# Kernel optimization log

Hardware: AMD Instinct MI355X
Metric: run time of the kernel (lower is better)

The kernel has to match this reference:

```python
import jax, jax.numpy as jnp
import numpy as np

B, L, DM, H = 1, 2048, 3072, 24
D = DM // H            # 128 head dim
MLP = 4 * DM           # 12288
EPS = 1e-6


def setup_inputs() -> dict:
    key = jax.random.key(0)
    ks = jax.random.split(key, 12)
    s = lambda fan_in: 1.0 / np.sqrt(fan_in)
    return {
        "x": jax.random.normal(ks[0], (B, L, DM), jnp.float32),
        "vec": jax.random.normal(ks[1], (B, DM), jnp.float32),
        "pe": jax.random.normal(ks[2], (1, 1, L, D // 2, 2, 2), jnp.float32),
        # Modulation linear: dim -> 3*dim
        "mod_w": jax.random.normal(ks[3], (DM, 3 * DM), jnp.float32) * s(DM),
        "mod_b": jnp.zeros((3 * DM,), jnp.float32),
        # linear1: dim -> 3*dim + mlp
        "lin1_w": jax.random.normal(ks[4], (DM, 3 * DM + MLP), jnp.float32) * s(DM),
        "lin1_b": jnp.zeros((3 * DM + MLP,), jnp.float32),
        # linear2: dim + mlp -> dim
        "lin2_w": jax.random.normal(ks[5], (DM + MLP, DM), jnp.float32) * s(DM + MLP),
        "lin2_b": jnp.zeros((DM,), jnp.float32),
        # QKNorm RMS scales (per head_dim)
        "q_scale": jnp.ones((D,), jnp.float32),
        "k_scale": jnp.ones((D,), jnp.float32),
    }


def _rms_norm(t, scale):
    # RMSNorm over last dim (head_dim), eps 1e-6
    rrms = jax.lax.rsqrt(jnp.mean(jnp.square(t), axis=-1, keepdims=True) + EPS)
    return t * rrms * scale


def _apply_rope(t, pe):
    # t: (B,H,L,D); pe: (1,1,L,D/2,2,2) as in flux apply_rope
    t2 = t.reshape(B, H, L, D // 2, 1, 2)
    out = pe[..., 0] * t2[..., 0] + pe[..., 1] * t2[..., 1]  # (B,H,L,D/2,2)
    return out.reshape(B, H, L, D)


def reference(x, vec, pe, mod_w, mod_b, lin1_w, lin1_b, lin2_w, lin2_b, q_scale, k_scale):
    # Modulation: Linear(silu(vec)) -> shift, scale, gate, each (B,1,DM)
    mod = jax.nn.silu(vec) @ mod_w + mod_b
    shift, scale, gate = jnp.split(mod[:, None, :], 3, axis=-1)

    # pre_norm: LayerNorm without affine, eps 1e-6
    mu = jnp.mean(x, axis=-1, keepdims=True)
    var = jnp.mean(jnp.square(x - mu), axis=-1, keepdims=True)
    xn = (x - mu) * jax.lax.rsqrt(var + EPS)
    x_mod = (1.0 + scale) * xn + shift

    # fused QKV + MLP projection
    h = x_mod @ lin1_w + lin1_b
    qkv, mlp = h[..., : 3 * DM], h[..., 3 * DM :]
    qkv = qkv.reshape(B, L, 3, H, D).transpose(2, 0, 3, 1, 4)  # (3,B,H,L,D)
    q, k, v = qkv[0], qkv[1], qkv[2]

    q = _rms_norm(q, q_scale)
    k = _rms_norm(k, k_scale)
    q = _apply_rope(q, pe)
    k = _apply_rope(k, pe)

    # scaled dot-product attention (non-causal, SDPA default scale)
    scores = jnp.einsum("bhqd,bhkd->bhqk", q, k) * (1.0 / np.sqrt(D))
    attn = jax.nn.softmax(scores, axis=-1)
    o = jnp.einsum("bhqk,bhkd->bhqd", attn, v)
    o = o.transpose(0, 2, 1, 3).reshape(B, L, DM)  # B H L D -> B L (H D)

    out = jnp.concatenate([o, jax.nn.gelu(mlp, approximate=True)], axis=-1) @ lin2_w + lin2_b
    return x + gate * out
```

## Files before the change

kernel.cpp:

```cpp
#include <hip/hip_runtime.h>
#include <math.h>

#define LQ 2048
#define DMODEL 3072
#define NHEADS 24
#define DHEADC 128
#define NQKV 9216
#define NOUT1 21504
#define KIN2 15360
#define EPSV 1e-6f

typedef __attribute__((ext_vector_type(8))) short short8;
typedef __attribute__((ext_vector_type(4))) short short4v;
typedef __attribute__((ext_vector_type(4))) float f32x4;

__device__ __forceinline__ short f2bf(float f) {
  unsigned int u = __float_as_uint(f);
  unsigned int r = (u + 0x7fffu + ((u >> 16) & 1u)) >> 16;
  return (short)(unsigned short)r;
}

__device__ __forceinline__ float geluf(float v) {
  float inner = 0.7978845608028654f * (v + 0.044715f * v * v * v);
  return 0.5f * v * (1.0f + tanhf(inner));
}

__device__ __forceinline__ void async_ld16(void* lds, const void* g) {
  __builtin_amdgcn_global_load_lds(
      (const __attribute__((address_space(1))) unsigned int*)g,
      (__attribute__((address_space(3))) unsigned int*)lds, 16, 0, 0);
}

__global__ __launch_bounds__(256) void k_wconv(const float* __restrict__ w,
                                               short* __restrict__ wt,
                                               int K, int N) {
  __shared__ float tile[32][33];
  int bk = blockIdx.x * 32, bn = blockIdx.y * 32;
  int t = threadIdx.x;
  int r = t >> 3, c = (t & 7) * 4;
  float4 v = *reinterpret_cast<const float4*>(w + (size_t)(bk + r) * N + bn + c);
  tile[r][c + 0] = v.x; tile[r][c + 1] = v.y; tile[r][c + 2] = v.z; tile[r][c + 3] = v.w;
  __syncthreads();
  short4v o;
  o[0] = f2bf(tile[c + 0][r]); o[1] = f2bf(tile[c + 1][r]);
  o[2] = f2bf(tile[c + 2][r]); o[3] = f2bf(tile[c + 3][r]);
  *reinterpret_cast<short4v*>(wt + (size_t)(bn + r) * K + bk + c) = o;
}

__global__ __launch_bounds__(256) void k_modpart(const float* __restrict__ vec,
                                                 const float* __restrict__ mod_w,
                                                 float* __restrict__ partial) {
  __shared__ float sv[128];
  int t = threadIdx.x;
  int nb = blockIdx.x * 256;
  int kb = blockIdx.y * 128;
  if (t < 128) { float z = vec[kb + t]; sv[t] = z / (1.0f + expf(-z)); }
  __syncthreads();
  const float* wp = mod_w + (size_t)kb * NQKV + nb + t;
  float acc = 0.0f;
#pragma unroll 8
  for (int k = 0; k < 128; k++) acc += sv[k] * wp[(size_t)k * NQKV];
  partial[(size_t)blockIdx.y * NQKV + nb + t] = acc;
}

__global__ __launch_bounds__(256) void k_modred(const float* __restrict__ partial,
                                                const float* __restrict__ mod_b,
                                                float* __restrict__ modv) {
  int n = blockIdx.x * 256 + threadIdx.x;
  float acc = mod_b[n];
#pragma unroll
  for (int ky = 0; ky < 24; ky++) acc += partial[(size_t)ky * NQKV + n];
  modv[n] = acc;
}

__global__ __launch_bounds__(256) void k_ln(const float* __restrict__ x,
                                            const float* __restrict__ modv,
                                            short* __restrict__ xmod) {
  int l = blockIdx.x, t = threadIdx.x;
  const float* xr = x + (size_t)l * DMODEL;
  const float4* xr4 = (const float4*)xr;
  float4 vbuf[3];
  float s = 0.f, ss = 0.f;
#pragma unroll
  for (int i = 0; i < 3; i++) {
    float4 v = xr4[t + i * 256];
    vbuf[i] = v;
    s += v.x + v.y + v.z + v.w;
    ss += v.x * v.x + v.y * v.y + v.z * v.z + v.w * v.w;
  }
#pragma unroll
  for (int m = 32; m >= 1; m >>= 1) { s += __shfl_xor(s, m); ss += __shfl_xor(ss, m); }
  __shared__ float red[8];
  __shared__ float stats[2];
  int wave = t >> 6;
  if ((t & 63) == 0) { red[wave] = s; red[4 + wave] = ss; }
  __syncthreads();
  if (t == 0) {
    float st = red[0] + red[1] + red[2] + red[3];
    float sst = red[4] + red[5] + red[6] + red[7];
    float mu = st / DMODEL;
    float var = sst / DMODEL - mu * mu;
    stats[0] = mu; stats[1] = rsqrtf(var + EPSV);
  }
  __syncthreads();
  float mu = stats[0], rr = stats[1];
#pragma unroll
  for (int i = 0; i < 3; i++) {
    float4 v = vbuf[i];
    int c = (t + i * 256) * 4;
    short4v o;
    o[0] = f2bf((1.f + modv[DMODEL + c + 0]) * ((v.x - mu) * rr) + modv[c + 0]);
    o[1] = f2bf((1.f + modv[DMODEL + c + 1]) * ((v.y - mu) * rr) + modv[c + 1]);
    o[2] = f2bf((1.f + modv[DMODEL + c + 2]) * ((v.z - mu) * rr) + modv[c + 2]);
    o[3] = f2bf((1.f + modv[DMODEL + c + 3]) * ((v.w - mu) * rr) + modv[c + 3]);
    *(short4v*)(xmod + (size_t)l * DMODEL + c) = o;
  }
}

#define G1_NT 48
#define G1_NITER 24

__device__ __forceinline__ void ldA4(short8 af[4][2], const short* ldsA, int rbase,
                                     int lrow, const int* kOff) {
#pragma unroll
  for (int m = 0; m < 4; m++)
#pragma unroll
    for (int ks = 0; ks < 2; ks++)
      af[m][ks] = *(const short8*)&ldsA[(rbase + m * 16 + lrow) * 64 + kOff[ks]];
}

__device__ __forceinline__ void ldB2(short8 bfr[2][2], const short* ldsB, int rbase,
                                     int lrow, const int* kOff) {
#pragma unroll
  for (int n = 0; n < 2; n++)
#pragma unroll
    for (int ks = 0; ks < 2; ks++)
      bfr[n][ks] = *(const short8*)&ldsB[(rbase + n * 16 + lrow) * 64 + kOff[ks]];
}

__device__ __forceinline__ void stage_halfA(short* ldsT, const short* G, int rowbase,
                                            int tauB, int half, int wid, int srow, int sk) {
#pragma unroll
  for (int c = 0; c < 2; c++) {
    int j = c * 8 + wid;
    int row0 = ((j >> 3) << 7) + half * 64 + ((j & 7) << 3);
    const char* src = (const char*)G +
                      (size_t)(rowbase + row0 + srow) * (size_t)(DMODEL * 2) + tauB + sk;
    async_ld16(ldsT + row0 * 64, src);
  }
}

__device__ __forceinline__ void stage_halfB(short* ldsT, const short* G, int rowbase,
                                            int tauB, int half, int wid, int srow, int sk) {
#pragma unroll
  for (int c = 0; c < 2; c++) {
    int j = c * 8 + wid;
    int row0 = ((j >> 2) << 6) + half * 32 + ((j & 3) << 3);
    const char* src = (const char*)G +
                      (size_t)(rowbase + row0 + srow) * (size_t)(DMODEL * 2) + tauB + sk;
    async_ld16(ldsT + row0 * 64, src);
  }
}

#define SYNC_MFMA(mh, nh, VM)                                                       \
  do {                                                                              \
    if (VM) asm volatile("s_waitcnt vmcnt(6)" ::: "memory");                        \
    __builtin_amdgcn_s_barrier();                                                   \
    asm volatile("s_waitcnt lgkmcnt(0)" ::: "memory");                              \
    __builtin_amdgcn_sched_barrier(0);                                              \
    __builtin_amdgcn_s_setprio(1);                                                  \
    _Pragma("unroll") for (int m_ = 0; m_ < 4; m_++)                                \
      _Pragma("unroll") for (int n_ = 0; n_ < 2; n_++)                              \
        _Pragma("unroll") for (int k_ = 0; k_ < 2; k_++)                            \
          acc[(mh) * 4 + m_][(nh) * 2 + n_] =                                       \
              __builtin_amdgcn_mfma_f32_16x16x32_bf16(                              \
                  af[m_][k_], bfr[n_][k_], acc[(mh) * 4 + m_][(nh) * 2 + n_], 0, 0, 0); \
    __builtin_amdgcn_s_setprio(0);                                                  \
    __builtin_amdgcn_s_barrier();                                                   \
  } while (0)

#define G1_TB(tt) ((((tt) < G1_NT) ? (tt) : (G1_NT - 1)) * 128)

__global__ __launch_bounds__(512, 2) void k_gemm1_8p(const short* __restrict__ A,
                                                     const short* __restrict__ Bt,
                                                     const float* __restrict__ bias,
                                                     float* __restrict__ qraw,
                                                     float* __restrict__ kraw,
                                                     short* __restrict__ vt,
                                                     short* __restrict__ a2) {
  __shared__ __align__(16) short lds[2][2][256 * 64];
  int t = threadIdx.x;
  int wid = t >> 6, lane = t & 63;
  int bid = blockIdx.x;
  int swzb = (bid & 7) * 84 + (bid >> 3);
  int bm = (swzb & 7) << 8;
  int bn = (swzb >> 3) << 8;
  int wm_ = (wid >> 2) << 7;
  int wn_ = (wid & 3) << 6;
  int lrow = lane & 15;
  int swzx = (lane & 7) << 4;
  int kOff[2];
#pragma unroll
  for (int ks = 0; ks < 2; ks++) kOff[ks] = ((ks * 64 + (lane >> 4) * 16) ^ swzx) >> 1;
  int srow = lane >> 3;
  int sk = ((lane & 7) * 16) ^ (srow << 4);

  short* A0p = &lds[0][0][0];
  short* B0p = &lds[0][1][0];
  short* A1p = &lds[1][0][0];
  short* B1p = &lds[1][1][0];

  f32x4 zero = {0.f, 0.f, 0.f, 0.f};
  f32x4 acc[8][4];
#pragma unroll
  for (int i = 0; i < 8; i++)
#pragma unroll
    for (int j = 0; j < 4; j++) acc[i][j] = zero;
  short8 af[4][2], bfr[2][2];

  stage_halfA(A0p, A, bm, 0, 0, wid, srow, sk);
  stage_halfA(A0p, A, bm, 0, 1, wid, srow, sk);
  stage_halfB(B0p, Bt, bn, 0, 0, wid, srow, sk);
  stage_halfB(B0p, Bt, bn, 0, 1, wid, srow, sk);
  stage_halfA(A1p, A, bm, 128, 0, wid, srow, sk);
  stage_halfB(B1p, Bt, bn, 128, 1, wid, srow, sk);
  stage_halfA(A1p, A, bm, 128, 1, wid, srow, sk);
  asm volatile("s_waitcnt vmcnt(6)" ::: "memory");
  __builtin_amdgcn_s_barrier();

#pragma unroll 1
  for (int it = 0; it < G1_NITER; ++it) {
    int T = it * 2;
    ldA4(af, A0p, wm_, lrow, kOff);
    ldB2(bfr, B0p, wn_, lrow, kOff);
    stage_halfB(B1p, Bt, bn, G1_TB(T + 1), 0, wid, srow, sk);
    SYNC_MFMA(0, 0, 0);
    ldB2(bfr, B0p, wn_ + 32, lrow, kOff);
    stage_halfA(A0p, A, bm, G1_TB(T + 2), 0, wid, srow, sk);
    SYNC_MFMA(0, 1, 0);
    ldA4(af, A0p, wm_ + 64, lrow, kOff);
    stage_halfB(B0p, Bt, bn, G1_TB(T + 2), 1, wid, srow, sk);
    SYNC_MFMA(1, 1, 0);
    ldB2(bfr, B0p, wn_, lrow, kOff);
    stage_halfA(A0p, A, bm, G1_TB(T + 2), 1, wid, srow, sk);
    SYNC_MFMA(1, 0, 1);
    ldA4(af, A1p, wm_, lrow, kOff);
    ldB2(bfr, B1p, wn_, lrow, kOff);
    stage_halfB(B0p, Bt, bn, G1_TB(T + 2), 0, wid, srow, sk);
    SYNC_MFMA(0, 0, 0);
    ldB2(bfr, B1p, wn_ + 32, lrow, kOff);
    stage_halfA(A1p, A, bm, G1_TB(T + 3), 0, wid, srow, sk);
    SYNC_MFMA(0, 1, 0);
    ldA4(af, A1p, wm_ + 64, lrow, kOff);
    stage_halfB(B1p, Bt, bn, G1_TB(T + 3), 1, wid, srow, sk);
    SYNC_MFMA(1, 1, 0);
    ldB2(bfr, B1p, wn_, lrow, kOff);
    stage_halfA(A1p, A, bm, G1_TB(T + 3), 1, wid, srow, sk);
    SYNC_MFMA(1, 0, 1);
  }

  int r0 = bm + wm_ + ((lane >> 4) << 2);
  int c0 = bn + wn_ + lrow;
#pragma unroll
  for (int an = 0; an < 4; an++) {
    int col = c0 + an * 16;
    float bb = bias[col];
#pragma unroll
    for (int am = 0; am < 8; am++) {
#pragma unroll
      for (int r = 0; r < 4; r++) {
        float v = acc[am][an][r] + bb;
        int row = r0 + am * 16 + r;
        if (col < NQKV) {
          int s = col / DMODEL;
          int rem = col - s * DMODEL;
          int hh = rem >> 7, d = rem & 127;
          if (s == 0)      qraw[((size_t)hh * LQ + row) * DHEADC + d] = v;
          else if (s == 1) kraw[((size_t)hh * LQ + row) * DHEADC + d] = v;
          else             vt[((size_t)hh * DHEADC + d) * LQ + row] = f2bf(v);
        } else {
          a2[(size_t)row * KIN2 + DMODEL + (col - NQKV)] = f2bf(geluf(v));
        }
      }
    }
  }
}

__global__ __launch_bounds__(256) void k_qkprep(const float* __restrict__ qraw,
                                                const float* __restrict__ kraw,
                                                const float* __restrict__ pe,
                                                const float* __restrict__ q_scale,
                                                const float* __restrict__ k_scale,
                                                short* __restrict__ qn,
                                                short* __restrict__ kn) {
  int wave = threadIdx.x >> 6, lane = threadIdx.x & 63;
  int l = blockIdx.x * 4 + wave;
  int h = blockIdx.y;
  int isK = blockIdx.z;
  const float* src = (isK ? kraw : qraw) + ((size_t)h * LQ + l) * DHEADC;
  const float* sc  = isK ? k_scale : q_scale;
  short* dst = (isK ? kn : qn) + ((size_t)h * LQ + l) * DHEADC;
  float2 tv = *(const float2*)(src + lane * 2);
  float ssq = tv.x * tv.x + tv.y * tv.y;
#pragma unroll
  for (int m = 1; m < 64; m <<= 1) ssq += __shfl_xor(ssq, m);
  float rr = rsqrtf(ssq * (1.0f / 128.0f) + EPSV);
  float t0 = tv.x * rr * sc[lane * 2];
  float t1 = tv.y * rr * sc[lane * 2 + 1];
  float4 p4 = *(const float4*)(pe + ((size_t)l * 64 + lane) * 4);
  float o0 = p4.x * t0 + p4.y * t1;
  float o1 = p4.z * t0 + p4.w * t1;
  if (!isK) { o0 *= 0.08838834764831845f; o1 *= 0.08838834764831845f; }
  dst[lane * 2] = f2bf(o0);
  dst[lane * 2 + 1] = f2bf(o1);
}

__global__ __launch_bounds__(256) void k_flash(const short* __restrict__ qn,
                                               const short* __restrict__ kn,
                                               const short* __restrict__ vt,
                                               short* __restrict__ a2) {
  __shared__ short Qs[128][136];
  __shared__ short Ks[32][136];
  __shared__ short Vs[128][40];
  __shared__ short Ps[4][32][40];
  int t = threadIdx.x;
  int qb = blockIdx.x * 128, h = blockIdx.y;
  int wave = t >> 6, lane = t & 63;
  int lrow = lane & 15, lko = (lane >> 4) * 8;
  int wm = wave * 32;
  const short* qbase = qn + ((size_t)h * LQ + qb) * DHEADC;
#pragma unroll
  for (int i = 0; i < 8; i++) {
    int idx = i * 256 + t;
    int row = idx >> 4, c = (idx & 15) * 8;
    *(short8*)&Qs[row][c] = *(const short8*)(qbase + (size_t)row * DHEADC + c);
  }
  f32x4 zero = {0.f, 0.f, 0.f, 0.f};
  f32x4 oacc[2][8];
#pragma unroll
  for (int i = 0; i < 2; i++)
#pragma unroll
    for (int j = 0; j < 8; j++) oacc[i][j] = zero;
  float mI[2][4], lI[2][4];
#pragma unroll
  for (int i = 0; i < 2; i++)
#pragma unroll
    for (int r = 0; r < 4; r++) { mI[i][r] = -1e30f; lI[i][r] = 0.f; }
  __syncthreads();
  for (int kt = 0; kt < 64; kt++) {
    int krow0 = kt * 32;
#pragma unroll
    for (int i = 0; i < 2; i++) {
      int idx = i * 256 + t;
      int row = idx >> 4, c = (idx & 15) * 8;
      *(short8*)&Ks[row][c] = *(const short8*)(kn + ((size_t)h * LQ + krow0 + row) * DHEADC + c);
    }
#pragma unroll
    for (int i = 0; i < 2; i++) {
      int idx = i * 256 + t;
      int d = idx >> 2, c = (idx & 3) * 8;
      *(short8*)&Vs[d][c] = *(const short8*)(vt + ((size_t)h * DHEADC + d) * LQ + krow0 + c);
    }
    __syncthreads();
    f32x4 sacc[2][2];
#pragma unroll
    for (int i = 0; i < 2; i++)
#pragma unroll
      for (int j = 0; j < 2; j++) sacc[i][j] = zero;
#pragma unroll
    for (int kk = 0; kk < 4; kk++) {
      short8 qa[2], kb[2];
#pragma unroll
      for (int i = 0; i < 2; i++) qa[i] = *(const short8*)&Qs[wm + i * 16 + lrow][kk * 32 + lko];
#pragma unroll
      for (int j = 0; j < 2; j++) kb[j] = *(const short8*)&Ks[j * 16 + lrow][kk * 32 + lko];
#pragma unroll
      for (int i = 0; i < 2; i++)
#pragma unroll
        for (int j = 0; j < 2; j++)
          sacc[i][j] = __builtin_amdgcn_mfma_f32_16x16x32_bf16(qa[i], kb[j], sacc[i][j], 0, 0, 0);
    }
#pragma unroll
    for (int i = 0; i < 2; i++) {
      float al[4];
#pragma unroll
      for (int r = 0; r < 4; r++) {
        float mx = fmaxf(sacc[i][0][r], sacc[i][1][r]);
#pragma unroll
        for (int m = 1; m < 16; m <<= 1) mx = fmaxf(mx, __shfl_xor(mx, m));
        float mnew = fmaxf(mI[i][r], mx);
        float alpha = exp2f((mI[i][r] - mnew) * 1.4426950408889634f);
        float p0 = exp2f((sacc[i][0][r] - mnew) * 1.4426950408889634f);
        float p1 = exp2f((sacc[i][1][r] - mnew) * 1.4426950408889634f);
        sacc[i][0][r] = p0; sacc[i][1][r] = p1;
        float rs = p0 + p1;
#pragma unroll
        for (int m = 1; m < 16; m <<= 1) rs += __shfl_xor(rs, m);
        lI[i][r] = lI[i][r] * alpha + rs;
        mI[i][r] = mnew;
        al[r] = alpha;
      }
#pragma unroll
      for (int j = 0; j < 8; j++) {
        f32x4 o = oacc[i][j];
        o[0] *= al[0]; o[1] *= al[1]; o[2] *= al[2]; o[3] *= al[3];
        oacc[i][j] = o;
      }
#pragma unroll
      for (int j = 0; j < 2; j++)
#pragma unroll
        for (int r = 0; r < 4; r++)
          Ps[wave][i * 16 + (lane >> 4) * 4 + r][j * 16 + lrow] = f2bf(sacc[i][j][r]);
    }
    short8 pa[2];
#pragma unroll
    for (int i = 0; i < 2; i++) pa[i] = *(const short8*)&Ps[wave][i * 16 + lrow][lko];
#pragma unroll
    for (int j = 0; j < 8; j++) {
      short8 vb = *(const short8*)&Vs[j * 16 + lrow][lko];
#pragma unroll
      for (int i = 0; i < 2; i++)
        oacc[i][j] = __builtin_amdgcn_mfma_f32_16x16x32_bf16(pa[i], vb, oacc[i][j], 0, 0, 0);
    }
    __syncthreads();
  }
#pragma unroll
  for (int i = 0; i < 2; i++) {
    float inv[4];
#pragma unroll
    for (int r = 0; r < 4; r++) inv[r] = 1.0f / lI[i][r];
#pragma unroll
    for (int j = 0; j < 8; j++) {
#pragma unroll
      for (int r = 0; r < 4; r++) {
        int row = qb + wm + i * 16 + (lane >> 4) * 4 + r;
        int col = h * DHEADC + j * 16 + lrow;
        a2[(size_t)row * KIN2 + col] = f2bf(oacc[i][j][r] * inv[r]);
      }
    }
  }
}

__global__ __launch_bounds__(256) void k_gemm2(const short* __restrict__ A,
                                               const short* __restrict__ Bt,
                                               const float* __restrict__ bias,
                                               const float* __restrict__ x,
                                               const float* __restrict__ gate,
                                               float* __restrict__ out) {
  __shared__ __align__(16) short As[128 * 32];
  __shared__ __align__(16) short Bs[128 * 32];
  const int K = KIN2;
  int t = threadIdx.x;
  int bm = blockIdx.x * 128, bn = blockIdx.y * 128;
  int wave = t >> 6, lane = t & 63;
  int wm = (wave >> 1) * 64, wn = (wave & 1) * 64;
  int lrow = lane & 15, lko = (lane >> 4) * 8;
  int srow = wave * 16 + (lane >> 2);
  int scol = (lane & 3) * 8;
  const short* ga0 = A + (size_t)(bm + srow) * K + scol;
  const short* ga1 = ga0 + (size_t)64 * K;
  const short* gb0 = Bt + (size_t)(bn + srow) * K + scol;
  const short* gb1 = gb0 + (size_t)64 * K;
  short* la0 = As + wave * 512;
  short* la1 = As + 64 * 32 + wave * 512;
  short* lb0 = Bs + wave * 512;
  short* lb1 = Bs + 64 * 32 + wave * 512;
  f32x4 zero = {0.f, 0.f, 0.f, 0.f};
  f32x4 acc[4][4];
#pragma unroll
  for (int i = 0; i < 4; i++)
#pragma unroll
    for (int j = 0; j < 4; j++) acc[i][j] = zero;
  for (int k0 = 0; k0 < K; k0 += 32) {
    __syncthreads();
    async_ld16(la0, ga0 + k0);
    async_ld16(la1, ga1 + k0);
    async_ld16(lb0, gb0 + k0);
    async_ld16(lb1, gb1 + k0);
    __syncthreads();
    short8 af[4], bfr[4];
#pragma unroll
    for (int i = 0; i < 4; i++) af[i] = *(const short8*)&As[(wm + i * 16 + lrow) * 32 + lko];
#pragma unroll
    for (int j = 0; j < 4; j++) bfr[j] = *(const short8*)&Bs[(wn + j * 16 + lrow) * 32 + lko];
#pragma unroll
    for (int i = 0; i < 4; i++)
#pragma unroll
      for (int j = 0; j < 4; j++)
        acc[i][j] = __builtin_amdgcn_mfma_f32_16x16x32_bf16(af[i], bfr[j], acc[i][j], 0, 0, 0);
  }
  int r0 = bm + wm + ((lane >> 4) << 2);
  int c0 = bn + wn + lrow;
#pragma unroll
  for (int j = 0; j < 4; j++) {
    int col = c0 + j * 16;
    float bb = bias[col];
    float g = gate[col];
#pragma unroll
    for (int i = 0; i < 4; i++) {
#pragma unroll
      for (int r = 0; r < 4; r++) {
        int row = r0 + i * 16 + r;
        float v = acc[i][j][r] + bb;
        out[(size_t)row * DMODEL + col] = x[(size_t)row * DMODEL + col] + g * v;
      }
    }
  }
}

extern "C" void kernel_launch(void* const* d_in, const int* in_sizes, int n_in,
                              void* d_out, int out_size, void* d_ws, size_t ws_size,
                              hipStream_t stream) {
  (void)in_sizes; (void)n_in; (void)out_size; (void)ws_size;
  const float* x       = (const float*)d_in[0];
  const float* vec     = (const float*)d_in[1];
  const float* pe      = (const float*)d_in[2];
  const float* mod_w   = (const float*)d_in[3];
  const float* mod_b   = (const float*)d_in[4];
  const float* lin1_w  = (const float*)d_in[5];
  const float* lin1_b  = (const float*)d_in[6];
  const float* lin2_w  = (const float*)d_in[7];
  const float* lin2_b  = (const float*)d_in[8];
  const float* q_scale = (const float*)d_in[9];
  const float* k_scale = (const float*)d_in[10];
  float* out = (float*)d_out;

  char* base = (char*)d_ws;
  size_t off = 0;
  auto carve = [&](size_t bytes) -> void* {
    void* q = base + off;
    off += (bytes + 255) & ~(size_t)255;
    return q;
  };
  short* W1t  = (short*)carve((size_t)NOUT1 * DMODEL * 2);
  short* xmod = (short*)carve((size_t)LQ * DMODEL * 2);
  float* qraw = (float*)carve((size_t)NHEADS * LQ * DHEADC * 4);
  float* kraw = (float*)carve((size_t)NHEADS * LQ * DHEADC * 4);
  short* qnb  = (short*)carve((size_t)NHEADS * LQ * DHEADC * 2);
  short* knb  = (short*)carve((size_t)NHEADS * LQ * DHEADC * 2);
  short* vtb  = (short*)carve((size_t)NHEADS * LQ * DHEADC * 2);
  short* a2   = (short*)carve((size_t)LQ * KIN2 * 2);
  float* modv = (float*)carve((size_t)NQKV * 4);
  float* part = (float*)carve((size_t)24 * NQKV * 4);

  k_wconv<<<dim3(DMODEL / 32, NOUT1 / 32), 256, 0, stream>>>(lin1_w, W1t, DMODEL, NOUT1);
  k_modpart<<<dim3(NQKV / 256, 24), 256, 0, stream>>>(vec, mod_w, part);
  k_modred<<<NQKV / 256, 256, 0, stream>>>(part, mod_b, modv);
  k_ln<<<LQ, 256, 0, stream>>>(x, modv, xmod);
  k_gemm1_8p<<<dim3((LQ / 256) * (NOUT1 / 256)), 512, 0, stream>>>(xmod, W1t, lin1_b,
                                                                   qraw, kraw, vtb, a2);
  k_wconv<<<dim3(KIN2 / 32, DMODEL / 32), 256, 0, stream>>>(lin2_w, W1t, KIN2, DMODEL);
  k_qkprep<<<dim3(LQ / 4, NHEADS, 2), 256, 0, stream>>>(qraw, kraw, pe, q_scale, k_scale, qnb, knb);
  k_flash<<<dim3(LQ / 128, NHEADS), 256, 0, stream>>>(qnb, knb, vtb, a2);
  k_gemm2<<<dim3(LQ / 128, DMODEL / 128), 256, 0, stream>>>(a2, W1t, lin2_b, x, modv + 2 * DMODEL, out);
}
```

Before: 1.628 ms.

## Replace naive second GEMM with pipelined 256x256 split-K kernel plus reduction

Swaps the simple 128x128, single-buffered lin2 GEMM for a copy of the 8-wave, double-buffered, swizzled-LDS pipeline already used for the first GEMM. K is split four ways so the grid has 384 blocks. Each split writes fp32 partials into workspace that reuses the dead xmod/q/k buffers. A separate elementwise kernel then sums the partials and applies bias, gate and the residual add. The aim is much higher MFMA utilisation on the largest remaining GEMM, paid for with about 100MB of extra partial-sum traffic and one more launch.

```diff
diff --git a/kernel.cpp b/kernel.cpp
--- a/kernel.cpp
+++ b/kernel.cpp
@@ -119,6 +119,9 @@
 
 #define G1_NT 48
 #define G1_NITER 24
+#define G2_KC 3840
+#define G2_NT 60
+#define G2_NITER 30
 
 __device__ __forceinline__ void ldA4(short8 af[4][2], const short* ldsA, int rbase,
                                      int lrow, const int* kOff) {
@@ -139,25 +142,27 @@
 }
 
 __device__ __forceinline__ void stage_halfA(short* ldsT, const short* G, int rowbase,
-                                            int tauB, int half, int wid, int srow, int sk) {
+                                            int tauB, int half, int wid, int srow, int sk,
+                                            size_t strideB) {
 #pragma unroll
   for (int c = 0; c < 2; c++) {
     int j = c * 8 + wid;
     int row0 = ((j >> 3) << 7) + half * 64 + ((j & 7) << 3);
     const char* src = (const char*)G +
-                      (size_t)(rowbase + row0 + srow) * (size_t)(DMODEL * 2) + tauB + sk;
+                      (size_t)(rowbase + row0 + srow) * strideB + tauB + sk;
     async_ld16(ldsT + row0 * 64, src);
   }
 }
 
 __device__ __forceinline__ void stage_halfB(short* ldsT, const short* G, int rowbase,
-                                            int tauB, int half, int wid, int srow, int sk) {
+                                            int tauB, int half, int wid, int srow, int sk,
+                                            size_t strideB) {
 #pragma unroll
   for (int c = 0; c < 2; c++) {
     int j = c * 8 + wid;
     int row0 = ((j >> 2) << 6) + half * 32 + ((j & 3) << 3);
     const char* src = (const char*)G +
-                      (size_t)(rowbase + row0 + srow) * (size_t)(DMODEL * 2) + tauB + sk;
+                      (size_t)(rowbase + row0 + srow) * strideB + tauB + sk;
     async_ld16(ldsT + row0 * 64, src);
   }
 }
@@ -180,6 +185,7 @@
   } while (0)
 
 #define G1_TB(tt) ((((tt) < G1_NT) ? (tt) : (G1_NT - 1)) * 128)
+#define G2_TB(tt) ((((tt) < G2_NT) ? (tt) : (G2_NT - 1)) * 128)
 
 __global__ __launch_bounds__(512, 2) void k_gemm1_8p(const short* __restrict__ A,
                                                      const short* __restrict__ Bt,
@@ -204,6 +210,7 @@
   for (int ks = 0; ks < 2; ks++) kOff[ks] = ((ks * 64 + (lane >> 4) * 16) ^ swzx) >> 1;
   int srow = lane >> 3;
   int sk = ((lane & 7) * 16) ^ (srow << 4);
+  const size_t strA = (size_t)(DMODEL * 2);
 
   short* A0p = &lds[0][0][0];
   short* B0p = &lds[0][1][0];
@@ -218,13 +225,13 @@
     for (int j = 0; j < 4; j++) acc[i][j] = zero;
   short8 af[4][2], bfr[2][2];
 
-  stage_halfA(A0p, A, bm, 0, 0, wid, srow, sk);
-  stage_halfA(A0p, A, bm, 0, 1, wid, srow, sk);
-  stage_halfB(B0p, Bt, bn, 0, 0, wid, srow, sk);
-  stage_halfB(B0p, Bt, bn, 0, 1, wid, srow, sk);
-  stage_halfA(A1p, A, bm, 128, 0, wid, srow, sk);
-  stage_halfB(B1p, Bt, bn, 128, 1, wid, srow, sk);
-  stage_halfA(A1p, A, bm, 128, 1, wid, srow, sk);
+  stage_halfA(A0p, A, bm, 0, 0, wid, srow, sk, strA);
+  stage_halfA(A0p, A, bm, 0, 1, wid, srow, sk, strA);
+  stage_halfB(B0p, Bt, bn, 0, 0, wid, srow, sk, strA);
+  stage_halfB(B0p, Bt, bn, 0, 1, wid, srow, sk, strA);
+  stage_halfA(A1p, A, bm, 128, 0, wid, srow, sk, strA);
+  stage_halfB(B1p, Bt, bn, 128, 1, wid, srow, sk, strA);
+  stage_halfA(A1p, A, bm, 128, 1, wid, srow, sk, strA);
   asm volatile("s_waitcnt vmcnt(6)" ::: "memory");
   __builtin_amdgcn_s_barrier();
 
@@ -233,29 +240,29 @@
     int T = it * 2;
     ldA4(af, A0p, wm_, lrow, kOff);
     ldB2(bfr, B0p, wn_, lrow, kOff);
-    stage_halfB(B1p, Bt, bn, G1_TB(T + 1), 0, wid, srow, sk);
+    stage_halfB(B1p, Bt, bn, G1_TB(T + 1), 0, wid, srow, sk, strA);
     SYNC_MFMA(0, 0, 0);
     ldB2(bfr, B0p, wn_ + 32, lrow, kOff);
-    stage_halfA(A0p, A, bm, G1_TB(T + 2), 0, wid, srow, sk);
+    stage_halfA(A0p, A, bm, G1_TB(T + 2), 0, wid, srow, sk, strA);
     SYNC_MFMA(0, 1, 0);
     ldA4(af, A0p, wm_ + 64, lrow, kOff);
-    stage_halfB(B0p, Bt, bn, G1_TB(T + 2), 1, wid, srow, sk);
+    stage_halfB(B0p, Bt, bn, G1_TB(T + 2), 1, wid, srow, sk, strA);
     SYNC_MFMA(1, 1, 0);
     ldB2(bfr, B0p, wn_, lrow, kOff);
-    stage_halfA(A0p, A, bm, G1_TB(T + 2), 1, wid, srow, sk);
+    stage_halfA(A0p, A, bm, G1_TB(T + 2), 1, wid, srow, sk, strA);
     SYNC_MFMA(1, 0, 1);
     ldA4(af, A1p, wm_, lrow, kOff);
     ldB2(bfr, B1p, wn_, lrow, kOff);
-    stage_halfB(B0p, Bt, bn, G1_TB(T + 2), 0, wid, srow, sk);
+    stage_halfB(B0p, Bt, bn, G1_TB(T + 2), 0, wid, srow, sk, strA);
     SYNC_MFMA(0, 0, 0);
     ldB2(bfr, B1p, wn_ + 32, lrow, kOff);
-    stage_halfA(A1p, A, bm, G1_TB(T + 3), 0, wid, srow, sk);
+    stage_halfA(A1p, A, bm, G1_TB(T + 3), 0, wid, srow, sk, strA);
     SYNC_MFMA(0, 1, 0);
     ldA4(af, A1p, wm_ + 64, lrow, kOff);
-    stage_halfB(B1p, Bt, bn, G1_TB(T + 3), 1, wid, srow, sk);
+    stage_halfB(B1p, Bt, bn, G1_TB(T + 3), 1, wid, srow, sk, strA);
     SYNC_MFMA(1, 1, 0);
     ldB2(bfr, B1p, wn_, lrow, kOff);
-    stage_halfA(A1p, A, bm, G1_TB(T + 3), 1, wid, srow, sk);
+    stage_halfA(A1p, A, bm, G1_TB(T + 3), 1, wid, srow, sk, strA);
     SYNC_MFMA(1, 0, 1);
   }
 
@@ -284,6 +291,128 @@
       }
     }
   }
+}
+
+__global__ __launch_bounds__(512, 2) void k_gemm2_8p(const short* __restrict__ A,
+                                                     const short* __restrict__ Bt,
+                                                     float* __restrict__ part) {
+  __shared__ __align__(16) short lds[2][2][256 * 64];
+  int t = threadIdx.x;
+  int wid = t >> 6, lane = t & 63;
+  int bid = blockIdx.x;
+  int swzb = (bid & 7) * 48 + (bid >> 3);
+  int bmIdx = swzb & 7;
+  int g = swzb >> 3;
+  int bnIdx = g % 12;
+  int s = g / 12;
+  int bm = bmIdx << 8;
+  int bn = bnIdx << 8;
+  const short* Ab = A + (size_t)s * G2_KC;
+  const short* Bb = Bt + (size_t)s * G2_KC;
+  float* Pb = part + (size_t)s * LQ * DMODEL;
+  int wm_ = (wid >> 2) << 7;
+  int wn_ = (wid & 3) << 6;
+  int lrow = lane & 15;
+  int swzx = (lane & 7) << 4;
+  int kOff[2];
+#pragma unroll
+  for (int ks = 0; ks < 2; ks++) kOff[ks] = ((ks * 64 + (lane >> 4) * 16) ^ swzx) >> 1;
+  int srow = lane >> 3;
+  int sk = ((lane & 7) * 16) ^ (srow << 4);
+  const size_t strA = (size_t)(KIN2 * 2);
+
+  short* A0p = &lds[0][0][0];
+  short* B0p = &lds[0][1][0];
+  short* A1p = &lds[1][0][0];
+  short* B1p = &lds[1][1][0];
+
+  f32x4 zero = {0.f, 0.f, 0.f, 0.f};
+  f32x4 acc[8][4];
+#pragma unroll
+  for (int i = 0; i < 8; i++)
+#pragma unroll
+    for (int j = 0; j < 4; j++) acc[i][j] = zero;
+  short8 af[4][2], bfr[2][2];
+
+  stage_halfA(A0p, Ab, bm, 0, 0, wid, srow, sk, strA);
+  stage_halfA(A0p, Ab, bm, 0, 1, wid, srow, sk, strA);
+  stage_halfB(B0p, Bb, bn, 0, 0, wid, srow, sk, strA);
+  stage_halfB(B0p, Bb, bn, 0, 1, wid, srow, sk, strA);
+  stage_halfA(A1p, Ab, bm, 128, 0, wid, srow, sk, strA);
+  stage_halfB(B1p, Bb, bn, 128, 1, wid, srow, sk, strA);
+  stage_halfA(A1p, Ab, bm, 128, 1, wid, srow, sk, strA);
+  asm volatile("s_waitcnt vmcnt(6)" ::: "memory");
+  __builtin_amdgcn_s_barrier();
+
+#pragma unroll 1
+  for (int it = 0; it < G2_NITER; ++it) {
+    int T = it * 2;
+    ldA4(af, A0p, wm_, lrow, kOff);
+    ldB2(bfr, B0p, wn_, lrow, kOff);
+    stage_halfB(B1p, Bb, bn, G2_TB(T + 1), 0, wid, srow, sk, strA);
+    SYNC_MFMA(0, 0, 0);
+    ldB2(bfr, B0p, wn_ + 32, lrow, kOff);
+    stage_halfA(A0p, Ab, bm, G2_TB(T + 2), 0, wid, srow, sk, strA);
+    SYNC_MFMA(0, 1, 0);
+    ldA4(af, A0p, wm_ + 64, lrow, kOff);
+    stage_halfB(B0p, Bb, bn, G2_TB(T + 2), 1, wid, srow, sk, strA);
+    SYNC_MFMA(1, 1, 0);
+    ldB2(bfr, B0p, wn_, lrow, kOff);
+    stage_halfA(A0p, Ab, bm, G2_TB(T + 2), 1, wid, srow, sk, strA);
+    SYNC_MFMA(1, 0, 1);
+    ldA4(af, A1p, wm_, lrow, kOff);
+    ldB2(bfr, B1p, wn_, lrow, kOff);
+    stage_halfB(B0p, Bb, bn, G2_TB(T + 2), 0, wid, srow, sk, strA);
+    SYNC_MFMA(0, 0, 0);
+    ldB2(bfr, B1p, wn_ + 32, lrow, kOff);
+    stage_halfA(A1p, Ab, bm, G2_TB(T + 3), 0, wid, srow, sk, strA);
+    SYNC_MFMA(0, 1, 0);
+    ldA4(af, A1p, wm_ + 64, lrow, kOff);
+    stage_halfB(B1p, Bb, bn, G2_TB(T + 3), 1, wid, srow, sk, strA);
+    SYNC_MFMA(1, 1, 0);
+    ldB2(bfr, B1p, wn_, lrow, kOff);
+    stage_halfA(A1p, Ab, bm, G2_TB(T + 3), 1, wid, srow, sk, strA);
+    SYNC_MFMA(1, 0, 1);
+  }
+
+  int r0 = bm + wm_ + ((lane >> 4) << 2);
+  int c0 = bn + wn_ + lrow;
+#pragma unroll
+  for (int an = 0; an < 4; an++) {
+    int col = c0 + an * 16;
+#pragma unroll
+    for (int am = 0; am < 8; am++) {
+#pragma unroll
+      for (int r = 0; r < 4; r++) {
+        int row = r0 + am * 16 + r;
+        Pb[(size_t)row * DMODEL + col] = acc[am][an][r];
+      }
+    }
+  }
+}
+
+__global__ __launch_bounds__(256) void k_g2red(const float* __restrict__ part,
+                                               const float* __restrict__ bias,
+                                               const float* __restrict__ x,
+                                               const float* __restrict__ gate,
+                                               float* __restrict__ out) {
+  int idx = blockIdx.x * 256 + threadIdx.x;
+  int c4 = idx % (DMODEL / 4);
+  const float4* p4 = (const float4*)part;
+  const size_t st4 = (size_t)LQ * DMODEL / 4;
+  float4 s0 = p4[idx];
+  float4 s1 = p4[idx + st4];
+  float4 s2 = p4[idx + 2 * st4];
+  float4 s3 = p4[idx + 3 * st4];
+  float4 b4 = ((const float4*)bias)[c4];
+  float4 g4 = ((const float4*)gate)[c4];
+  float4 x4 = ((const float4*)x)[idx];
+  float4 o;
+  o.x = x4.x + g4.x * (b4.x + s0.x + s1.x + s2.x + s3.x);
+  o.y = x4.y + g4.y * (b4.y + s0.y + s1.y + s2.y + s3.y);
+  o.z = x4.z + g4.z * (b4.z + s0.z + s1.z + s2.z + s3.z);
+  o.w = x4.w + g4.w * (b4.w + s0.w + s1.w + s2.w + s3.w);
+  ((float4*)out)[idx] = o;
 }
 
 __global__ __launch_bounds__(256) void k_qkprep(const float* __restrict__ qraw,
@@ -436,73 +565,6 @@
         int row = qb + wm + i * 16 + (lane >> 4) * 4 + r;
         int col = h * DHEADC + j * 16 + lrow;
         a2[(size_t)row * KIN2 + col] = f2bf(oacc[i][j][r] * inv[r]);
-      }
-    }
-  }
-}
-
-__global__ __launch_bounds__(256) void k_gemm2(const short* __restrict__ A,
-                                               const short* __restrict__ Bt,
-                                               const float* __restrict__ bias,
-                                               const float* __restrict__ x,
-                                               const float* __restrict__ gate,
-                                               float* __restrict__ out) {
-  __shared__ __align__(16) short As[128 * 32];
-  __shared__ __align__(16) short Bs[128 * 32];
-  const int K = KIN2;
-  int t = threadIdx.x;
-  int bm = blockIdx.x * 128, bn = blockIdx.y * 128;
-  int wave = t >> 6, lane = t & 63;
-  int wm = (wave >> 1) * 64, wn = (wave & 1) * 64;
-  int lrow = lane & 15, lko = (lane >> 4) * 8;
-  int srow = wave * 16 + (lane >> 2);
-  int scol = (lane & 3) * 8;
-  const short* ga0 = A + (size_t)(bm + srow) * K + scol;
-  const short* ga1 = ga0 + (size_t)64 * K;
-  const short* gb0 = Bt + (size_t)(bn + srow) * K + scol;
-  const short* gb1 = gb0 + (size_t)64 * K;
-  short* la0 = As + wave * 512;
-  short* la1 = As + 64 * 32 + wave * 512;
-  short* lb0 = Bs + wave * 512;
-  short* lb1 = Bs + 64 * 32 + wave * 512;
-  f32x4 zero = {0.f, 0.f, 0.f, 0.f};
-  f32x4 acc[4][4];
-#pragma unroll
-  for (int i = 0; i < 4; i++)
-#pragma unroll
-    for (int j = 0; j < 4; j++) acc[i][j] = zero;
-  for (int k0 = 0; k0 < K; k0 += 32) {
-    __syncthreads();
-    async_ld16(la0, ga0 + k0);
-    async_ld16(la1, ga1 + k0);
-    async_ld16(lb0, gb0 + k0);
-    async_ld16(lb1, gb1 + k0);
-    __syncthreads();
-    short8 af[4], bfr[4];
-#pragma unroll
-    for (int i = 0; i < 4; i++) af[i] = *(const short8*)&As[(wm + i * 16 + lrow) * 32 + lko];
-#pragma unroll
-    for (int j = 0; j < 4; j++) bfr[j] = *(const short8*)&Bs[(wn + j * 16 + lrow) * 32 + lko];
-#pragma unroll
-    for (int i = 0; i < 4; i++)
-#pragma unroll
-      for (int j = 0; j < 4; j++)
-        acc[i][j] = __builtin_amdgcn_mfma_f32_16x16x32_bf16(af[i], bfr[j], acc[i][j], 0, 0, 0);
-  }
-  int r0 = bm + wm + ((lane >> 4) << 2);
-  int c0 = bn + wn + lrow;
-#pragma unroll
-  for (int j = 0; j < 4; j++) {
-    int col = c0 + j * 16;
-    float bb = bias[col];
-    float g = gate[col];
-#pragma unroll
-    for (int i = 0; i < 4; i++) {
-#pragma unroll
-      for (int r = 0; r < 4; r++) {
-        int row = r0 + i * 16 + r;
-        float v = acc[i][j][r] + bb;
-        out[(size_t)row * DMODEL + col] = x[(size_t)row * DMODEL + col] + g * v;
       }
     }
   }
@@ -542,6 +604,7 @@
   short* a2   = (short*)carve((size_t)LQ * KIN2 * 2);
   float* modv = (float*)carve((size_t)NQKV * 4);
   float* part = (float*)carve((size_t)24 * NQKV * 4);
+  float* g2part = (float*)xmod;
 
   k_wconv<<<dim3(DMODEL / 32, NOUT1 / 32), 256, 0, stream>>>(lin1_w, W1t, DMODEL, NOUT1);
   k_modpart<<<dim3(NQKV / 256, 24), 256, 0, stream>>>(vec, mod_w, part);
@@ -552,5 +615,7 @@
   k_wconv<<<dim3(KIN2 / 32, DMODEL / 32), 256, 0, stream>>>(lin2_w, W1t, KIN2, DMODEL);
   k_qkprep<<<dim3(LQ / 4, NHEADS, 2), 256, 0, stream>>>(qraw, kraw, pe, q_scale, k_scale, qnb, knb);
   k_flash<<<dim3(LQ / 128, NHEADS), 256, 0, stream>>>(qnb, knb, vtb, a2);
-  k_gemm2<<<dim3(LQ / 128, DMODEL / 128), 256, 0, stream>>>(a2, W1t, lin2_b, x, modv + 2 * DMODEL, out);
-}
+  k_gemm2_8p<<<dim3(384), 512, 0, stream>>>(a2, W1t, g2part);
+  k_g2red<<<dim3((LQ * DMODEL / 4) / 256), 256, 0, stream>>>(g2part, lin2_b, x,
+                                                             modv + 2 * DMODEL, out);
+}
```

Measured after the change: 1.476 ms. 1.1x faster.
